# Kernel optimization log

Hardware: AMD Instinct MI355X
Metric: run time of the kernel (lower is better)

Reference implementation:

```python
import jax, jax.numpy as jnp
import numpy as np

B, T, D = 4, 4096, 768      # batch, tokens, n_embd
S = 1024                    # memory_slots (divides T -> adaptive pool == window mean)
K = 8                       # memory_topk
RW = 0.1                    # memory_retrieval_weight


def setup_inputs() -> dict:
    key = jax.random.key(0)
    ks = jax.random.split(key, 10)
    w = 1.0 / np.sqrt(D).astype(np.float32)
    return {
        "x": jax.random.normal(ks[0], (B, T, D), jnp.float32),
        "Wq": jax.random.normal(ks[1], (D, D), jnp.float32) * w,
        "bq": jnp.zeros((D,), jnp.float32),
        "Wk": jax.random.normal(ks[2], (D, D), jnp.float32) * w,
        "bk": jnp.zeros((D,), jnp.float32),
        "Wv": jax.random.normal(ks[3], (D, D), jnp.float32) * w,
        "bv": jnp.zeros((D,), jnp.float32),
        "Wp": jax.random.normal(ks[4], (D, D), jnp.float32) * w,
        "bp": jnp.zeros((D,), jnp.float32),
        "persistent_memory": jax.random.normal(ks[5], (S, D), jnp.float32),
    }


def reference(x, Wq, bq, Wk, bk, Wv, bv, Wp, bp, persistent_memory):
    # _build_memory_slots: adaptive_avg_pool1d to S slots; T % S == 0 so it is a window mean
    pooled = x.reshape(B, S, T // S, D).mean(axis=2)                    # [B,S,D]
    pers = jnp.broadcast_to(persistent_memory[None], (B, S, D))         # persistent bank
    slots = jnp.concatenate([pooled, pers], axis=1)                     # [B,2S,D]

    q = x @ Wq + bq                                                     # [B,T,D]
    k = slots @ Wk + bk                                                 # [B,2S,D]
    v = slots @ Wv + bv                                                 # [B,2S,D]

    scores = jnp.einsum('btd,bsd->bts', q, k) / jnp.sqrt(jnp.float32(D))  # [B,T,2S]
    top_s, top_i = jax.lax.top_k(scores, K)                             # [B,T,K]
    w = jax.nn.softmax(top_s, axis=-1)                                  # softmax over top-k only

    # gather top-k values: [B,T,K,D]
    vg = jnp.take_along_axis(v, top_i.reshape(B, T * K)[:, :, None], axis=1)
    vg = vg.reshape(B, T, K, D)
    retrieved = jnp.einsum('btk,btkd->btd', w, vg)                      # weighted combine

    return RW * (retrieved @ Wp + bp)                                   # proj * retrieval_weight
```

## Files before the change

kernel.cpp:

```cpp
#include <hip/hip_runtime.h>
#include <math.h>

#define BB 4
#define TT 4096
#define DD 768
#define SS 1024
#define S2 2048
#define KTOP 8
#define RWEIGHT 0.1f
#define TAU 2e-4f
#define AMB_CAP 128

typedef __attribute__((ext_vector_type(8))) _Float16 f16x8;
typedef __attribute__((ext_vector_type(4))) float f32x4;
typedef _Float16 f16;

__global__ __launch_bounds__(256) void build_pooled_all(
    const float* __restrict__ x, float* __restrict__ slots)
{
    int i = blockIdx.x * 256 + threadIdx.x;
    int s2 = i / DD;
    int d = i - s2 * DD;
    int b = s2 >> 10, s = s2 & 1023;
    const float* xb = x + (size_t)b * TT * DD + (size_t)(4 * s) * DD + d;
// ... 12 lines not shown
              : (blockIdx.z == 2) ? T2 : T3;
    __shared__ float t[32][33];
    int bx = blockIdx.x * 32, by = blockIdx.y * 32;
    int lx = threadIdx.x & 31, ly = threadIdx.x >> 5;
#pragma unroll
    for (int r = 0; r < 32; r += 8)
        t[ly + r][lx] = W[(size_t)(bx + ly + r) * 768 + by + lx];
    __syncthreads();
#pragma unroll
    for (int r = 0; r < 32; r += 8)
        WT[(size_t)(by + ly + r) * 768 + bx + lx] = t[lx][ly + r];
}

__global__ void zeroN(int* p) { p[threadIdx.x] = 0; }

__global__ __launch_bounds__(256) void producers(
    const float* __restrict__ xq, const float* __restrict__ aslots,
    const f16* __restrict__ aproj,
    const float* __restrict__ WqT, const float* __restrict__ WkT,
    const float* __restrict__ WvT, const float* __restrict__ WpT,
    const float* __restrict__ bq, const float* __restrict__ bk,
    const float* __restrict__ bv, const float* __restrict__ bp,
    f16* __restrict__ qh, f16* __restrict__ qm,
    f16* __restrict__ kh, f16* __restrict__ km,
    f16* __restrict__ v16, float* __restrict__ oproj,
    int n_q, int n_kv, int rowoff)
{
    __shared__ f16 LAh[4096], LAm[4096], LBh[4096], LBm[4096];
    const int tid = threadIdx.x;
    const int lane = tid & 63;
    const int wc = (tid >> 6) & 1;
    const int wr = (tid >> 7) & 1;

    int t = blockIdx.x, mode, bx, by;
    if (t < n_q) { mode = 0; bx = t % 6; by = t / 6; }
    else if (t < n_q + n_kv) { mode = 1; int u = t - n_q; bx = u % 6; by = u / 6; }
    else if (t < n_q + 2 * n_kv) { mode = 2; int u = t - n_q - n_kv; bx = u % 6; by = u / 6; }
    else { mode = 3; int u = t - n_q - 2 * n_kv; bx = u % 6; by = u / 6; }

    const int srow = tid >> 1, c0 = tid & 1;
    const int p0 = c0 ^ (srow & 3) ^ ((srow >> 2) & 1);
    const int wo0 = srow * 32 + p0 * 8, wo1 = wo0 ^ 16;
    const int csw = (((lane >> 4) ^ (lane & 3) ^ ((lane >> 2) & 1)) * 8);
    const int arow0 = by * 128;
    const size_t bn = (size_t)bx * 128;

    f32x4 acc[4][4];
#pragma unroll
    for (int i = 0; i < 4; ++i)
#pragma unroll
        for (int j = 0; j < 4; ++j) acc[i][j] = (f32x4){0.f, 0.f, 0.f, 0.f};

    const int orow0 = wr * 64 + (lane >> 4) * 4;
    const int ocol0 = wc * 64 + (lane & 15);

    if (mode <= 1) {
        const float* A  = (mode == 0) ? xq : aslots;
        const float* BT = (mode == 0) ? WqT : WkT;
        const float* bi = (mode == 0) ? bq : bk;
        f16* Ch = (mode == 0) ? qh : kh;
        f16* Cm = (mode == 0) ? qm : km;
        const int crow0 = ((mode == 0) ? 0 : rowoff) + arow0;
        const float* pa = A + (size_t)(arow0 + srow) * 768 + c0 * 8;
        const float* pb = BT + (bn + srow) * 768 + c0 * 8;

        for (int k0 = 0; k0 < 768; k0 += 32) {
            float4 a0 = *(const float4*)(pa + k0);
            float4 a1 = *(const float4*)(pa + k0 + 4);
            float4 a2 = *(const float4*)(pa + k0 + 16);
            float4 a3 = *(const float4*)(pa + k0 + 20);
            float4 b0 = *(const float4*)(pb + k0);
            float4 b1 = *(const float4*)(pb + k0 + 4);
            float4 b2 = *(const float4*)(pb + k0 + 16);
            float4 b3 = *(const float4*)(pb + k0 + 20);
            __syncthreads();
            {
                float av[16] = {a0.x, a0.y, a0.z, a0.w, a1.x, a1.y, a1.z, a1.w,
                                a2.x, a2.y, a2.z, a2.w, a3.x, a3.y, a3.z, a3.w};
                float bv2[16] = {b0.x, b0.y, b0.z, b0.w, b1.x, b1.y, b1.z, b1.w,
                                 b2.x, b2.y, b2.z, b2.w, b3.x, b3.y, b3.z, b3.w};
                f16x8 h, m;
#pragma unroll
                for (int j = 0; j < 8; ++j) {
                    f16 hh = (f16)av[j]; h[j] = hh; m[j] = (f16)(av[j] - (float)hh);
                }
                *(f16x8*)&LAh[wo0] = h; *(f16x8*)&LAm[wo0] = m;
#pragma unroll
                for (int j = 0; j < 8; ++j) {
                    f16 hh = (f16)av[j + 8]; h[j] = hh; m[j] = (f16)(av[j + 8] - (float)hh);
                }
                *(f16x8*)&LAh[wo1] = h; *(f16x8*)&LAm[wo1] = m;
#pragma unroll
                for (int j = 0; j < 8; ++j) {
                    f16 hh = (f16)bv2[j]; h[j] = hh; m[j] = (f16)(bv2[j] - (float)hh);
                }
                *(f16x8*)&LBh[wo0] = h; *(f16x8*)&LBm[wo0] = m;
#pragma unroll
                for (int j = 0; j < 8; ++j) {
                    f16 hh = (f16)bv2[j + 8]; h[j] = hh; m[j] = (f16)(bv2[j + 8] - (float)hh);
                }
                *(f16x8*)&LBh[wo1] = h; *(f16x8*)&LBm[wo1] = m;
            }
            __syncthreads();

            f16x8 fah[4], fam[4], fbh[4], fbm[4];
#pragma unroll
            for (int mi = 0; mi < 4; ++mi) {
                int off = (wr * 64 + mi * 16 + (lane & 15)) * 32 + csw;
                fah[mi] = *(const f16x8*)&LAh[off];
                fam[mi] = *(const f16x8*)&LAm[off];
            }
#pragma unroll
            for (int ni = 0; ni < 4; ++ni) {
                int off = (wc * 64 + ni * 16 + (lane & 15)) * 32 + csw;
                fbh[ni] = *(const f16x8*)&LBh[off];
                fbm[ni] = *(const f16x8*)&LBm[off];
            }
#pragma unroll
            for (int mi = 0; mi < 4; ++mi)
#pragma unroll
                for (int ni = 0; ni < 4; ++ni) {
                    acc[mi][ni] = __builtin_amdgcn_mfma_f32_16x16x32_f16(
                        fah[mi], fbh[ni], acc[mi][ni], 0, 0, 0);
                    acc[mi][ni] = __builtin_amdgcn_mfma_f32_16x16x32_f16(
                        fah[mi], fbm[ni], acc[mi][ni], 0, 0, 0);
                    acc[mi][ni] = __builtin_amdgcn_mfma_f32_16x16x32_f16(
                        fam[mi], fbh[ni], acc[mi][ni], 0, 0, 0);
                }
        }
#pragma unroll
        for (int mi = 0; mi < 4; ++mi)
#pragma unroll
            for (int ni = 0; ni < 4; ++ni) {
                size_t col = bn + ocol0 + ni * 16;
                float badd = bi[col];
                size_t rbase = (size_t)crow0 + orow0 + mi * 16;
#pragma unroll
                for (int r = 0; r < 4; ++r) {
                    float val = acc[mi][ni][r] + badd;
                    f16 h = (f16)val;
                    size_t idx = (rbase + r) * 768 + col;
                    Ch[idx] = h;
                    Cm[idx] = (f16)(val - (float)h);
                }
            }
    } else if (mode == 2) {
        const int crow0 = rowoff + arow0;
        const float* pa = aslots + (size_t)(arow0 + srow) * 768 + c0 * 8;
        const float* pb = WvT + (bn + srow) * 768 + c0 * 8;
        for (int k0 = 0; k0 < 768; k0 += 32) {
            float4 a0 = *(const float4*)(pa + k0);
            float4 a1 = *(const float4*)(pa + k0 + 4);
            float4 a2 = *(const float4*)(pa + k0 + 16);
            float4 a3 = *(const float4*)(pa + k0 + 20);
            float4 b0 = *(const float4*)(pb + k0);
            float4 b1 = *(const float4*)(pb + k0 + 4);
            float4 b2 = *(const float4*)(pb + k0 + 16);
            float4 b3 = *(const float4*)(pb + k0 + 20);
            __syncthreads();
            {
                f16x8 h;
                h[0] = (f16)a0.x; h[1] = (f16)a0.y; h[2] = (f16)a0.z; h[3] = (f16)a0.w;
                h[4] = (f16)a1.x; h[5] = (f16)a1.y; h[6] = (f16)a1.z; h[7] = (f16)a1.w;
                *(f16x8*)&LAh[wo0] = h;
                h[0] = (f16)a2.x; h[1] = (f16)a2.y; h[2] = (f16)a2.z; h[3] = (f16)a2.w;
                h[4] = (f16)a3.x; h[5] = (f16)a3.y; h[6] = (f16)a3.z; h[7] = (f16)a3.w;
                *(f16x8*)&LAh[wo1] = h;
                h[0] = (f16)b0.x; h[1] = (f16)b0.y; h[2] = (f16)b0.z; h[3] = (f16)b0.w;
                h[4] = (f16)b1.x; h[5] = (f16)b1.y; h[6] = (f16)b1.z; h[7] = (f16)b1.w;
                *(f16x8*)&LBh[wo0] = h;
                h[0] = (f16)b2.x; h[1] = (f16)b2.y; h[2] = (f16)b2.z; h[3] = (f16)b2.w;
                h[4] = (f16)b3.x; h[5] = (f16)b3.y; h[6] = (f16)b3.z; h[7] = (f16)b3.w;
                *(f16x8*)&LBh[wo1] = h;
            }
            __syncthreads();
            f16x8 fah[4], fbh[4];
#pragma unroll
            for (int mi = 0; mi < 4; ++mi)
                fah[mi] = *(const f16x8*)&LAh[(wr * 64 + mi * 16 + (lane & 15)) * 32 + csw];
#pragma unroll
            for (int ni = 0; ni < 4; ++ni)
                fbh[ni] = *(const f16x8*)&LBh[(wc * 64 + ni * 16 + (lane & 15)) * 32 + csw];
#pragma unroll
            for (int mi = 0; mi < 4; ++mi)
#pragma unroll
                for (int ni = 0; ni < 4; ++ni)
                    acc[mi][ni] = __builtin_amdgcn_mfma_f32_16x16x32_f16(
                        fah[mi], fbh[ni], acc[mi][ni], 0, 0, 0);
        }
#pragma unroll
        for (int mi = 0; mi < 4; ++mi)
#pragma unroll
            for (int ni = 0; ni < 4; ++ni) {
                size_t col = bn + ocol0 + ni * 16;
                float badd = bv[col];
                size_t rbase = (size_t)crow0 + orow0 + mi * 16;
#pragma unroll
                for (int r = 0; r < 4; ++r)
                    v16[(rbase + r) * 768 + col] = (f16)(acc[mi][ni][r] + badd);
            }
    } else {
        const f16* pa = aproj + (size_t)(arow0 + srow) * 768 + c0 * 8;
        const float* pb = WpT + (bn + srow) * 768 + c0 * 8;
        for (int k0 = 0; k0 < 768; k0 += 32) {
            f16x8 ah0 = *(const f16x8*)(pa + k0);
            f16x8 ah1 = *(const f16x8*)(pa + k0 + 16);
            float4 b0 = *(const float4*)(pb + k0);
            float4 b1 = *(const float4*)(pb + k0 + 4);
            float4 b2 = *(const float4*)(pb + k0 + 16);
            float4 b3 = *(const float4*)(pb + k0 + 20);
            __syncthreads();
            *(f16x8*)&LAh[wo0] = ah0;
            *(f16x8*)&LAh[wo1] = ah1;
            {
                f16x8 h;
                h[0] = (f16)b0.x; h[1] = (f16)b0.y; h[2] = (f16)b0.z; h[3] = (f16)b0.w;
                h[4] = (f16)b1.x; h[5] = (f16)b1.y; h[6] = (f16)b1.z; h[7] = (f16)b1.w;
                *(f16x8*)&LBh[wo0] = h;
                h[0] = (f16)b2.x; h[1] = (f16)b2.y; h[2] = (f16)b2.z; h[3] = (f16)b2.w;
                h[4] = (f16)b3.x; h[5] = (f16)b3.y; h[6] = (f16)b3.z; h[7] = (f16)b3.w;
                *(f16x8*)&LBh[wo1] = h;
            }
            __syncthreads();
            f16x8 fah[4], fbh[4];
#pragma unroll
            for (int mi = 0; mi < 4; ++mi)
                fah[mi] = *(const f16x8*)&LAh[(wr * 64 + mi * 16 + (lane & 15)) * 32 + csw];
#pragma unroll
            for (int ni = 0; ni < 4; ++ni)
                fbh[ni] = *(const f16x8*)&LBh[(wc * 64 + ni * 16 + (lane & 15)) * 32 + csw];
#pragma unroll
            for (int mi = 0; mi < 4; ++mi)
#pragma unroll
                for (int ni = 0; ni < 4; ++ni)
                    acc[mi][ni] = __builtin_amdgcn_mfma_f32_16x16x32_f16(
                        fah[mi], fbh[ni], acc[mi][ni], 0, 0, 0);
        }
#pragma unroll
        for (int mi = 0; mi < 4; ++mi)
#pragma unroll
            for (int ni = 0; ni < 4; ++ni) {
                size_t col = bn + ocol0 + ni * 16;
                float badd = RWEIGHT * bp[col];
                size_t rbase = (size_t)arow0 + orow0 + mi * 16;
#pragma unroll
                for (int r = 0; r < 4; ++r)
                    oproj[(rbase + r) * 768 + col] = RWEIGHT * acc[mi][ni][r] + badd;
            }
    }
}

__global__ __launch_bounds__(256) void scores_planes(
    const f16* __restrict__ qh, const f16* __restrict__ qm,
    const f16* __restrict__ kh, const f16* __restrict__ km,
    float* __restrict__ C, float alpha)
{
    __shared__ f16 LAh[4096], LAm[4096], LBh[4096], LBm[4096];
    const int tid = threadIdx.x;
    const int lane = tid & 63;
    const int wc = (tid >> 6) & 1;
    const int wr = (tid >> 7) & 1;
    const size_t bm = (size_t)blockIdx.y * 128;
    const size_t bn = (size_t)blockIdx.x * 128;

    f32x4 acc[4][4];
#pragma unroll
    for (int i = 0; i < 4; ++i)
#pragma unroll
        for (int j = 0; j < 4; ++j) acc[i][j] = (f32x4){0.f, 0.f, 0.f, 0.f};

    const int srow = tid >> 1, c0 = tid & 1;
    const int p0 = c0 ^ (srow & 3) ^ ((srow >> 2) & 1);
    const int wo0 = srow * 32 + p0 * 8, wo1 = wo0 ^ 16;
    const int csw = (((lane >> 4) ^ (lane & 3) ^ ((lane >> 2) & 1)) * 8);

    const f16* pah = qh + (bm + srow) * 768 + c0 * 8;
    const f16* pam = qm + (bm + srow) * 768 + c0 * 8;
    const f16* pbh = kh + (bn + srow) * 768 + c0 * 8;
    const f16* pbm = km + (bn + srow) * 768 + c0 * 8;

    for (int k0 = 0; k0 < 768; k0 += 32) {
        f16x8 ah0 = *(const f16x8*)(pah + k0);
        f16x8 ah1 = *(const f16x8*)(pah + k0 + 16);
        f16x8 am0 = *(const f16x8*)(pam + k0);
        f16x8 am1 = *(const f16x8*)(pam + k0 + 16);
        f16x8 bh0 = *(const f16x8*)(pbh + k0);
        f16x8 bh1 = *(const f16x8*)(pbh + k0 + 16);
        f16x8 bm0 = *(const f16x8*)(pbm + k0);
        f16x8 bm1 = *(const f16x8*)(pbm + k0 + 16);
        __syncthreads();
        *(f16x8*)&LAh[wo0] = ah0; *(f16x8*)&LAh[wo1] = ah1;
        *(f16x8*)&LAm[wo0] = am0; *(f16x8*)&LAm[wo1] = am1;
// ... 22 lines not shown
                    fah[mi], fbh[ni], acc[mi][ni], 0, 0, 0);
                acc[mi][ni] = __builtin_amdgcn_mfma_f32_16x16x32_f16(
                    fah[mi], fbm[ni], acc[mi][ni], 0, 0, 0);
                acc[mi][ni] = __builtin_amdgcn_mfma_f32_16x16x32_f16(
                    fam[mi], fbh[ni], acc[mi][ni], 0, 0, 0);
            }
    }

    const int orow0 = wr * 64 + (lane >> 4) * 4;
    const int ocol0 = wc * 64 + (lane & 15);
#pragma unroll
    for (int mi = 0; mi < 4; ++mi)
#pragma unroll
        for (int ni = 0; ni < 4; ++ni) {
            size_t col = bn + ocol0 + ni * 16;
            size_t rbase = bm + orow0 + mi * 16;
#pragma unroll
            for (int r = 0; r < 4; ++r)
                C[(rbase + r) * S2 + col] = alpha * acc[mi][ni][r];
        }
}

__global__ __launch_bounds__(256) void select_combine(
    const float* __restrict__ scores, const f16* __restrict__ v16,
    f16* __restrict__ retrc, int gbase,
    int* __restrict__ amb_count, int* __restrict__ amb_grow,
    int* __restrict__ cand, float* __restrict__ oldw, f16* __restrict__ vsave)
{
    const int lane = threadIdx.x & 63;
    const int wave = threadIdx.x >> 6;
    const int row = blockIdx.x * 4 + wave;

    const float* srow = scores + (size_t)row * S2;
    float vals[32];
#pragma unroll
    for (int i = 0; i < 32; ++i) vals[i] = srow[lane + (i << 6)];

    float topv[16]; int topi[16];
    bool amb = false;
    int nr = 9;
    for (int r = 0; r < 16; ++r) {
        if (r >= nr) break;
        float bvv = -3.4e38f; int bii = 0x7fffffff;
#pragma unroll
        for (int i = 0; i < 32; ++i)
            if (vals[i] > bvv) { bvv = vals[i]; bii = lane + (i << 6); }
#pragma unroll
        for (int off = 32; off > 0; off >>= 1) {
            float ov = __shfl_xor(bvv, off);
            int   oi = __shfl_xor(bii, off);
            if (ov > bvv || (ov == bvv && oi < bii)) { bvv = ov; bii = oi; }
        }
        topv[r] = bvv; topi[r] = bii;
        if ((bii & 63) == lane) vals[bii >> 6] = -3.4e38f;
        if (r == 8) {
            amb = (topv[7] - topv[8]) < TAU;
            if (amb) nr = 16;
        }
    }

    float m = topv[0], w[KTOP], sum = 0.f;
#pragma unroll
    for (int r = 0; r < KTOP; ++r) { w[r] = expf(topv[r] - m); sum += w[r]; }
    float inv = 1.f / sum;
#pragma unroll
    for (int r = 0; r < KTOP; ++r) w[r] *= inv;

    if (amb) {
        int idx = 0;
        if (lane == 0) idx = atomicAdd(amb_count, 1);
        idx = __shfl(idx, 0);
        if (idx < AMB_CAP) {
            if (lane == 0) amb_grow[idx] = gbase + row;
            if (lane < 16) cand[idx * 16 + lane] = topi[lane];
            if (lane < KTOP) oldw[idx * KTOP + lane] = w[lane];
            f16* vs = vsave + (size_t)idx * 16 * 768;
            for (int cc = lane; cc < 16 * 96; cc += 64) {
                int cr = cc / 96, ch = cc - cr * 96;
                *(f16x8*)&vs[(size_t)cr * 768 + ch * 8] =
                    *(const f16x8*)&v16[(size_t)topi[cr] * 768 + ch * 8];
            }
        }
    }

    for (int c = lane; c < 96; c += 64) {
        float o[8] = {0, 0, 0, 0, 0, 0, 0, 0};
#pragma unroll
        for (int r = 0; r < KTOP; ++r) {
            f16x8 vv = *(const f16x8*)&v16[(size_t)topi[r] * 768 + c * 8];
#pragma unroll
            for (int j = 0; j < 8; ++j) o[j] += w[r] * (float)vv[j];
        }
        f16x8 hx;
#pragma unroll
        for (int j = 0; j < 8; ++j) hx[j] = (f16)o[j];
        *(f16x8*)&retrc[(size_t)row * 768 + c * 8] = hx;
    }
}

__global__ __launch_bounds__(256) void fixA(
    const int* __restrict__ amb_count, const int* __restrict__ amb_grow,
    const float* __restrict__ x, const float* __restrict__ Wq,
    const float* __restrict__ bq, double* __restrict__ q64buf)
{
    int n = *amb_count; if (n > AMB_CAP) n = AMB_CAP;
    const int i = blockIdx.y;
    if (i >= n) return;
    const int tid = threadIdx.x;
    const int jl = tid & 63;
    const int ks = tid >> 6;
    const int j = blockIdx.x * 64 + jl;
    const int grow = amb_grow[i];
// ... 201 lines not shown
    const float inv_sqrt_d = (float)(1.0 / sqrt((double)DD));
    const size_t TD  = (size_t)TT * DD;
    const size_t SD  = (size_t)SS * DD;
    const size_t WSZ = (size_t)DD * DD;

    float* p = ws;
    float* WqT = p; p += WSZ;
    float* WkT = p; p += WSZ;
    float* WvT = p; p += WSZ;
    float* WpT = p; p += WSZ;
    float* slots_all = p; p += (size_t)BB * SD;
    f16* qh = (f16*)p; p += TD / 2;
    f16* qm = (f16*)p; p += TD / 2;
    f16* kh = (f16*)p; p += SD;
    f16* km = (f16*)p; p += SD;
    f16* v16 = (f16*)p; p += SD;
    f16* retrA = (f16*)p; p += TD / 2;
    f16* retrB = (f16*)p; p += TD / 2;
    double* q64buf = (double*)p; p += (size_t)AMB_CAP * DD * 2;
    double* ubuf   = (double*)p; p += (size_t)AMB_CAP * DD * 2;
    double* bkqbuf = (double*)p; p += AMB_CAP * 2;
    int* cand = (int*)p; p += (size_t)AMB_CAP * 16;
    float* oldw = p; p += (size_t)AMB_CAP * KTOP;
    f16* vsave = (f16*)p; p += (size_t)AMB_CAP * 16 * DD / 2;
    float* dret = p; p += (size_t)AMB_CAP * DD;
    int* ambc = (int*)p; p += 64;
    int* ambgrow = (int*)p; p += AMB_CAP;
    float* scores = p;
    size_t used = (size_t)(p - ws);

    long tc = TT;
    while (tc > 512 && (used + (size_t)tc * S2) * 4 > ws_size) tc >>= 1;

    transpose_all<<<dim3(24, 24, 4), 256, 0, stream>>>(
        Wq, Wk, Wv, Wp, WqT, WkT, WvT, WpT);
    zeroN<<<1, 64, 0, stream>>>(ambc);
    build_pooled_all<<<(BB * SS * DD) / 256, 256, 0, stream>>>(x, slots_all);

    producers<<<96, 256, 0, stream>>>(
        nullptr, pm, nullptr, WqT, WkT, WvT, WpT, bq, bk, bv, bp,
        qh, qm, kh, km, v16, nullptr, 0, 48, SS);

    for (int b = 0; b < BB; ++b) {
        const float* xb = x + (size_t)b * TD;
        const float* slots_b = slots_all + (size_t)b * SD;
        f16* rcur = (b & 1) ? retrB : retrA;
        f16* rprev = (b & 1) ? retrA : retrB;
        int np = b ? 192 : 0;

        producers<<<288 + np, 256, 0, stream>>>(
            xb, slots_b, rprev, WqT, WkT, WvT, WpT, bq, bk, bv, bp,
            qh, qm, kh, km, v16, out + (size_t)(b - 1) * TD, 192, 48, 0);

        for (long t0 = 0; t0 < TT; t0 += tc) {
            scores_planes<<<dim3(16, tc / 128), 256, 0, stream>>>(
                qh + (size_t)t0 * DD, qm + (size_t)t0 * DD, kh, km,
                scores, inv_sqrt_d);
            select_combine<<<tc / 4, 256, 0, stream>>>(
                scores, v16, rcur + (size_t)t0 * DD, b * TT + (int)t0,
                ambc, ambgrow, cand, oldw, vsave);
        }
    }

    f16* rlast = ((BB - 1) & 1) ? retrB : retrA;
    producers<<<192, 256, 0, stream>>>(
        nullptr, nullptr, rlast, WqT, WkT, WvT, WpT, bq, bk, bv, bp,
        qh, qm, kh, km, v16, out + (size_t)(BB - 1) * TD, 0, 0, 0);

    fixA<<<dim3(12, AMB_CAP), 256, 0, stream>>>(ambc, ambgrow, x, Wq, bq, q64buf);
    fixB<<<dim3(12, AMB_CAP), 256, 0, stream>>>(ambc, WkT, bk, q64buf, ubuf, bkqbuf);
    fixC<<<AMB_CAP, 256, 0, stream>>>(ambc, ambgrow, x, pm, cand, oldw,
                                      ubuf, bkqbuf, vsave, dret);
    fixD<<<dim3(12, AMB_CAP), 256, 0, stream>>>(ambc, ambgrow, dret, Wp, out);
}
```

Baseline: 648.5 us.

## Fuse select/combine with next-batch producers and scores with projection into mega-kernels

Splits the producer GEMM variants into device tile functions and builds two heterogeneous mega-kernels. One runs top-k selection and combine for batch b-1 alongside the Q/K/V producers for batch b. The other runs the score GEMM for batch b alongside the output projection of batch b-1. This software-pipelines the batches across fewer launches so independent work fills the GPU together. The V buffer is now double-buffered and the persistent-memory V is written to both copies. The adaptive chunking of the scores buffer by workspace size is removed, so the full T×2S scores buffer is now assumed to fit.

```diff
diff --git a/kernel.cpp b/kernel.cpp
--- a/kernel.cpp
+++ b/kernel.cpp
@@ -50,268 +50,297 @@
 
 __global__ void zeroN(int* p) { p[threadIdx.x] = 0; }
 
-__global__ __launch_bounds__(256) void producers(
-    const float* __restrict__ xq, const float* __restrict__ aslots,
-    const f16* __restrict__ aproj,
-    const float* __restrict__ WqT, const float* __restrict__ WkT,
-    const float* __restrict__ WvT, const float* __restrict__ WpT,
-    const float* __restrict__ bq, const float* __restrict__ bk,
-    const float* __restrict__ bv, const float* __restrict__ bp,
-    f16* __restrict__ qh, f16* __restrict__ qm,
-    f16* __restrict__ kh, f16* __restrict__ km,
-    f16* __restrict__ v16, float* __restrict__ oproj,
-    int n_q, int n_kv, int rowoff)
-{
-    __shared__ f16 LAh[4096], LAm[4096], LBh[4096], LBm[4096];
+__device__ __forceinline__ void tile_split_prod(
+    const float* __restrict__ A, int arow0,
+    const float* __restrict__ BT, int bncol,
+    const float* __restrict__ bias,
+    f16* __restrict__ Ch, f16* __restrict__ Cm, int crow0,
+    f16* LAh, f16* LAm, f16* LBh, f16* LBm)
+{
     const int tid = threadIdx.x;
     const int lane = tid & 63;
     const int wc = (tid >> 6) & 1;
     const int wr = (tid >> 7) & 1;
-
-    int t = blockIdx.x, mode, bx, by;
-    if (t < n_q) { mode = 0; bx = t % 6; by = t / 6; }
-    else if (t < n_q + n_kv) { mode = 1; int u = t - n_q; bx = u % 6; by = u / 6; }
-    else if (t < n_q + 2 * n_kv) { mode = 2; int u = t - n_q - n_kv; bx = u % 6; by = u / 6; }
-    else { mode = 3; int u = t - n_q - 2 * n_kv; bx = u % 6; by = u / 6; }
-
     const int srow = tid >> 1, c0 = tid & 1;
     const int p0 = c0 ^ (srow & 3) ^ ((srow >> 2) & 1);
     const int wo0 = srow * 32 + p0 * 8, wo1 = wo0 ^ 16;
     const int csw = (((lane >> 4) ^ (lane & 3) ^ ((lane >> 2) & 1)) * 8);
-    const int arow0 = by * 128;
-    const size_t bn = (size_t)bx * 128;
+    const size_t bn = (size_t)bncol;
 
     f32x4 acc[4][4];
 #pragma unroll
     for (int i = 0; i < 4; ++i)
 #pragma unroll
         for (int j = 0; j < 4; ++j) acc[i][j] = (f32x4){0.f, 0.f, 0.f, 0.f};
+
+    const float* pa = A + (size_t)(arow0 + srow) * 768 + c0 * 8;
+    const float* pb = BT + (bn + srow) * 768 + c0 * 8;
+
+    for (int k0 = 0; k0 < 768; k0 += 32) {
+        float4 a0 = *(const float4*)(pa + k0);
+        float4 a1 = *(const float4*)(pa + k0 + 4);
+        float4 a2 = *(const float4*)(pa + k0 + 16);
+        float4 a3 = *(const float4*)(pa + k0 + 20);
+        float4 b0 = *(const float4*)(pb + k0);
+        float4 b1 = *(const float4*)(pb + k0 + 4);
+        float4 b2 = *(const float4*)(pb + k0 + 16);
+        float4 b3 = *(const float4*)(pb + k0 + 20);
+        __syncthreads();
+        {
+            float av[16] = {a0.x, a0.y, a0.z, a0.w, a1.x, a1.y, a1.z, a1.w,
+                            a2.x, a2.y, a2.z, a2.w, a3.x, a3.y, a3.z, a3.w};
+            float bv2[16] = {b0.x, b0.y, b0.z, b0.w, b1.x, b1.y, b1.z, b1.w,
+                             b2.x, b2.y, b2.z, b2.w, b3.x, b3.y, b3.z, b3.w};
+            f16x8 h, m;
+#pragma unroll
+            for (int j = 0; j < 8; ++j) {
+                f16 hh = (f16)av[j]; h[j] = hh; m[j] = (f16)(av[j] - (float)hh);
+            }
+            *(f16x8*)&LAh[wo0] = h; *(f16x8*)&LAm[wo0] = m;
+#pragma unroll
+            for (int j = 0; j < 8; ++j) {
+                f16 hh = (f16)av[j + 8]; h[j] = hh; m[j] = (f16)(av[j + 8] - (float)hh);
+            }
+            *(f16x8*)&LAh[wo1] = h; *(f16x8*)&LAm[wo1] = m;
+#pragma unroll
+            for (int j = 0; j < 8; ++j) {
+                f16 hh = (f16)bv2[j]; h[j] = hh; m[j] = (f16)(bv2[j] - (float)hh);
+            }
+            *(f16x8*)&LBh[wo0] = h; *(f16x8*)&LBm[wo0] = m;
+#pragma unroll
+            for (int j = 0; j < 8; ++j) {
+                f16 hh = (f16)bv2[j + 8]; h[j] = hh; m[j] = (f16)(bv2[j + 8] - (float)hh);
+            }
+            *(f16x8*)&LBh[wo1] = h; *(f16x8*)&LBm[wo1] = m;
+        }
+        __syncthreads();
+
+        f16x8 fah[4], fam[4], fbh[4], fbm[4];
+#pragma unroll
+        for (int mi = 0; mi < 4; ++mi) {
+            int off = (wr * 64 + mi * 16 + (lane & 15)) * 32 + csw;
+            fah[mi] = *(const f16x8*)&LAh[off];
+            fam[mi] = *(const f16x8*)&LAm[off];
+        }
+#pragma unroll
+        for (int ni = 0; ni < 4; ++ni) {
+            int off = (wc * 64 + ni * 16 + (lane & 15)) * 32 + csw;
+            fbh[ni] = *(const f16x8*)&LBh[off];
+            fbm[ni] = *(const f16x8*)&LBm[off];
+        }
+#pragma unroll
+        for (int mi = 0; mi < 4; ++mi)
+#pragma unroll
+            for (int ni = 0; ni < 4; ++ni) {
+                acc[mi][ni] = __builtin_amdgcn_mfma_f32_16x16x32_f16(
+                    fah[mi], fbh[ni], acc[mi][ni], 0, 0, 0);
+                acc[mi][ni] = __builtin_amdgcn_mfma_f32_16x16x32_f16(
+                    fah[mi], fbm[ni], acc[mi][ni], 0, 0, 0);
+                acc[mi][ni] = __builtin_amdgcn_mfma_f32_16x16x32_f16(
+                    fam[mi], fbh[ni], acc[mi][ni], 0, 0, 0);
+            }
+    }
 
     const int orow0 = wr * 64 + (lane >> 4) * 4;
     const int ocol0 = wc * 64 + (lane & 15);
-
-    if (mode <= 1) {
-        const float* A  = (mode == 0) ? xq : aslots;
-        const float* BT = (mode == 0) ? WqT : WkT;
-        const float* bi = (mode == 0) ? bq : bk;
-        f16* Ch = (mode == 0) ? qh : kh;
-        f16* Cm = (mode == 0) ? qm : km;
-        const int crow0 = ((mode == 0) ? 0 : rowoff) + arow0;
-        const float* pa = A + (size_t)(arow0 + srow) * 768 + c0 * 8;
-        const float* pb = BT + (bn + srow) * 768 + c0 * 8;
-
-        for (int k0 = 0; k0 < 768; k0 += 32) {
-            float4 a0 = *(const float4*)(pa + k0);
-            float4 a1 = *(const float4*)(pa + k0 + 4);
-            float4 a2 = *(const float4*)(pa + k0 + 16);
-            float4 a3 = *(const float4*)(pa + k0 + 20);
-            float4 b0 = *(const float4*)(pb + k0);
-            float4 b1 = *(const float4*)(pb + k0 + 4);
-            float4 b2 = *(const float4*)(pb + k0 + 16);
-            float4 b3 = *(const float4*)(pb + k0 + 20);
-            __syncthreads();
-            {
-                float av[16] = {a0.x, a0.y, a0.z, a0.w, a1.x, a1.y, a1.z, a1.w,
-                                a2.x, a2.y, a2.z, a2.w, a3.x, a3.y, a3.z, a3.w};
-                float bv2[16] = {b0.x, b0.y, b0.z, b0.w, b1.x, b1.y, b1.z, b1.w,
-                                 b2.x, b2.y, b2.z, b2.w, b3.x, b3.y, b3.z, b3.w};
-                f16x8 h, m;
-#pragma unroll
-                for (int j = 0; j < 8; ++j) {
-                    f16 hh = (f16)av[j]; h[j] = hh; m[j] = (f16)(av[j] - (float)hh);
-                }
-                *(f16x8*)&LAh[wo0] = h; *(f16x8*)&LAm[wo0] = m;
-#pragma unroll
-                for (int j = 0; j < 8; ++j) {
-                    f16 hh = (f16)av[j + 8]; h[j] = hh; m[j] = (f16)(av[j + 8] - (float)hh);
-                }
-                *(f16x8*)&LAh[wo1] = h; *(f16x8*)&LAm[wo1] = m;
-#pragma unroll
-                for (int j = 0; j < 8; ++j) {
-                    f16 hh = (f16)bv2[j]; h[j] = hh; m[j] = (f16)(bv2[j] - (float)hh);
-                }
-                *(f16x8*)&LBh[wo0] = h; *(f16x8*)&LBm[wo0] = m;
-#pragma unroll
-                for (int j = 0; j < 8; ++j) {
-                    f16 hh = (f16)bv2[j + 8]; h[j] = hh; m[j] = (f16)(bv2[j + 8] - (float)hh);
-                }
-                *(f16x8*)&LBh[wo1] = h; *(f16x8*)&LBm[wo1] = m;
-            }
-            __syncthreads();
-
-            f16x8 fah[4], fam[4], fbh[4], fbm[4];
-#pragma unroll
-            for (int mi = 0; mi < 4; ++mi) {
-                int off = (wr * 64 + mi * 16 + (lane & 15)) * 32 + csw;
-                fah[mi] = *(const f16x8*)&LAh[off];
-                fam[mi] = *(const f16x8*)&LAm[off];
-            }
-#pragma unroll
-            for (int ni = 0; ni < 4; ++ni) {
-                int off = (wc * 64 + ni * 16 + (lane & 15)) * 32 + csw;
-                fbh[ni] = *(const f16x8*)&LBh[off];
-                fbm[ni] = *(const f16x8*)&LBm[off];
-            }
-#pragma unroll
-            for (int mi = 0; mi < 4; ++mi)
-#pragma unroll
-                for (int ni = 0; ni < 4; ++ni) {
-                    acc[mi][ni] = __builtin_amdgcn_mfma_f32_16x16x32_f16(
-                        fah[mi], fbh[ni], acc[mi][ni], 0, 0, 0);
-                    acc[mi][ni] = __builtin_amdgcn_mfma_f32_16x16x32_f16(
-                        fah[mi], fbm[ni], acc[mi][ni], 0, 0, 0);
-                    acc[mi][ni] = __builtin_amdgcn_mfma_f32_16x16x32_f16(
-                        fam[mi], fbh[ni], acc[mi][ni], 0, 0, 0);
-                }
-        }
-#pragma unroll
-        for (int mi = 0; mi < 4; ++mi)
-#pragma unroll
-            for (int ni = 0; ni < 4; ++ni) {
-                size_t col = bn + ocol0 + ni * 16;
-                float badd = bi[col];
-                size_t rbase = (size_t)crow0 + orow0 + mi * 16;
-#pragma unroll
-                for (int r = 0; r < 4; ++r) {
-                    float val = acc[mi][ni][r] + badd;
-                    f16 h = (f16)val;
-                    size_t idx = (rbase + r) * 768 + col;
-                    Ch[idx] = h;
-                    Cm[idx] = (f16)(val - (float)h);
-                }
-            }
-    } else if (mode == 2) {
-        const int crow0 = rowoff + arow0;
-        const float* pa = aslots + (size_t)(arow0 + srow) * 768 + c0 * 8;
-        const float* pb = WvT + (bn + srow) * 768 + c0 * 8;
-        for (int k0 = 0; k0 < 768; k0 += 32) {
-            float4 a0 = *(const float4*)(pa + k0);
-            float4 a1 = *(const float4*)(pa + k0 + 4);
-            float4 a2 = *(const float4*)(pa + k0 + 16);
-            float4 a3 = *(const float4*)(pa + k0 + 20);
-            float4 b0 = *(const float4*)(pb + k0);
-            float4 b1 = *(const float4*)(pb + k0 + 4);
-            float4 b2 = *(const float4*)(pb + k0 + 16);
-            float4 b3 = *(const float4*)(pb + k0 + 20);
-            __syncthreads();
-            {
-                f16x8 h;
-                h[0] = (f16)a0.x; h[1] = (f16)a0.y; h[2] = (f16)a0.z; h[3] = (f16)a0.w;
-                h[4] = (f16)a1.x; h[5] = (f16)a1.y; h[6] = (f16)a1.z; h[7] = (f16)a1.w;
-                *(f16x8*)&LAh[wo0] = h;
-                h[0] = (f16)a2.x; h[1] = (f16)a2.y; h[2] = (f16)a2.z; h[3] = (f16)a2.w;
-                h[4] = (f16)a3.x; h[5] = (f16)a3.y; h[6] = (f16)a3.z; h[7] = (f16)a3.w;
-                *(f16x8*)&LAh[wo1] = h;
-                h[0] = (f16)b0.x; h[1] = (f16)b0.y; h[2] = (f16)b0.z; h[3] = (f16)b0.w;
-                h[4] = (f16)b1.x; h[5] = (f16)b1.y; h[6] = (f16)b1.z; h[7] = (f16)b1.w;
-                *(f16x8*)&LBh[wo0] = h;
-                h[0] = (f16)b2.x; h[1] = (f16)b2.y; h[2] = (f16)b2.z; h[3] = (f16)b2.w;
-                h[4] = (f16)b3.x; h[5] = (f16)b3.y; h[6] = (f16)b3.z; h[7] = (f16)b3.w;
-                *(f16x8*)&LBh[wo1] = h;
-            }
-            __syncthreads();
-            f16x8 fah[4], fbh[4];
-#pragma unroll
-            for (int mi = 0; mi < 4; ++mi)
-                fah[mi] = *(const f16x8*)&LAh[(wr * 64 + mi * 16 + (lane & 15)) * 32 + csw];
-#pragma unroll
-            for (int ni = 0; ni < 4; ++ni)
-                fbh[ni] = *(const f16x8*)&LBh[(wc * 64 + ni * 16 + (lane & 15)) * 32 + csw];
-#pragma unroll
-            for (int mi = 0; mi < 4; ++mi)
-#pragma unroll
-                for (int ni = 0; ni < 4; ++ni)
-                    acc[mi][ni] = __builtin_amdgcn_mfma_f32_16x16x32_f16(
-                        fah[mi], fbh[ni], acc[mi][ni], 0, 0, 0);
-        }
-#pragma unroll
-        for (int mi = 0; mi < 4; ++mi)
-#pragma unroll
-            for (int ni = 0; ni < 4; ++ni) {
-                size_t col = bn + ocol0 + ni * 16;
-                float badd = bv[col];
-                size_t rbase = (size_t)crow0 + orow0 + mi * 16;
-#pragma unroll
-                for (int r = 0; r < 4; ++r)
-                    v16[(rbase + r) * 768 + col] = (f16)(acc[mi][ni][r] + badd);
-            }
-    } else {
-        const f16* pa = aproj + (size_t)(arow0 + srow) * 768 + c0 * 8;
-        const float* pb = WpT + (bn + srow) * 768 + c0 * 8;
-        for (int k0 = 0; k0 < 768; k0 += 32) {
-            f16x8 ah0 = *(const f16x8*)(pa + k0);
-            f16x8 ah1 = *(const f16x8*)(pa + k0 + 16);
-            float4 b0 = *(const float4*)(pb + k0);
-            float4 b1 = *(const float4*)(pb + k0 + 4);
-            float4 b2 = *(const float4*)(pb + k0 + 16);
-            float4 b3 = *(const float4*)(pb + k0 + 20);
-            __syncthreads();
-            *(f16x8*)&LAh[wo0] = ah0;
-            *(f16x8*)&LAh[wo1] = ah1;
-            {
-                f16x8 h;
-                h[0] = (f16)b0.x; h[1] = (f16)b0.y; h[2] = (f16)b0.z; h[3] = (f16)b0.w;
-                h[4] = (f16)b1.x; h[5] = (f16)b1.y; h[6] = (f16)b1.z; h[7] = (f16)b1.w;
-                *(f16x8*)&LBh[wo0] = h;
-                h[0] = (f16)b2.x; h[1] = (f16)b2.y; h[2] = (f16)b2.z; h[3] = (f16)b2.w;
-                h[4] = (f16)b3.x; h[5] = (f16)b3.y; h[6] = (f16)b3.z; h[7] = (f16)b3.w;
-                *(f16x8*)&LBh[wo1] = h;
-            }
-            __syncthreads();
-            f16x8 fah[4], fbh[4];
-#pragma unroll
-            for (int mi = 0; mi < 4; ++mi)
-                fah[mi] = *(const f16x8*)&LAh[(wr * 64 + mi * 16 + (lane & 15)) * 32 + csw];
-#pragma unroll
-            for (int ni = 0; ni < 4; ++ni)
-                fbh[ni] = *(const f16x8*)&LBh[(wc * 64 + ni * 16 + (lane & 15)) * 32 + csw];
-#pragma unroll
-            for (int mi = 0; mi < 4; ++mi)
-#pragma unroll
-                for (int ni = 0; ni < 4; ++ni)
-                    acc[mi][ni] = __builtin_amdgcn_mfma_f32_16x16x32_f16(
-                        fah[mi], fbh[ni], acc[mi][ni], 0, 0, 0);
-        }
-#pragma unroll
-        for (int mi = 0; mi < 4; ++mi)
-#pragma unroll
-            for (int ni = 0; ni < 4; ++ni) {
-                size_t col = bn + ocol0 + ni * 16;
-                float badd = RWEIGHT * bp[col];
-                size_t rbase = (size_t)arow0 + orow0 + mi * 16;
-#pragma unroll
-                for (int r = 0; r < 4; ++r)
-                    oproj[(rbase + r) * 768 + col] = RWEIGHT * acc[mi][ni][r] + badd;
-            }
-    }
-}
-
-__global__ __launch_bounds__(256) void scores_planes(
-    const f16* __restrict__ qh, const f16* __restrict__ qm,
-    const f16* __restrict__ kh, const f16* __restrict__ km,
-    float* __restrict__ C, float alpha)
-{
-    __shared__ f16 LAh[4096], LAm[4096], LBh[4096], LBm[4096];
+#pragma unroll
+    for (int mi = 0; mi < 4; ++mi)
+#pragma unroll
+        for (int ni = 0; ni < 4; ++ni) {
+            size_t col = bn + ocol0 + ni * 16;
+            float badd = bias[col];
+            size_t rbase = (size_t)crow0 + orow0 + mi * 16;
+#pragma unroll
+            for (int r = 0; r < 4; ++r) {
+                float val = acc[mi][ni][r] + badd;
+                f16 h = (f16)val;
+                size_t idx = (rbase + r) * 768 + col;
+                Ch[idx] = h;
+                Cm[idx] = (f16)(val - (float)h);
+            }
+        }
+}
+
+__device__ __forceinline__ void tile_f32A_f16O(
+    const float* __restrict__ A, int arow0,
+    const float* __restrict__ BT, int bncol,
+    const float* __restrict__ bias,
+    f16* __restrict__ Co, int crow0, f16* LA, f16* LB)
+{
     const int tid = threadIdx.x;
     const int lane = tid & 63;
     const int wc = (tid >> 6) & 1;
     const int wr = (tid >> 7) & 1;
-    const size_t bm = (size_t)blockIdx.y * 128;
-    const size_t bn = (size_t)blockIdx.x * 128;
-
-    f32x4 acc[4][4];
-#pragma unroll
-    for (int i = 0; i < 4; ++i)
-#pragma unroll
-        for (int j = 0; j < 4; ++j) acc[i][j] = (f32x4){0.f, 0.f, 0.f, 0.f};
-
     const int srow = tid >> 1, c0 = tid & 1;
     const int p0 = c0 ^ (srow & 3) ^ ((srow >> 2) & 1);
     const int wo0 = srow * 32 + p0 * 8, wo1 = wo0 ^ 16;
     const int csw = (((lane >> 4) ^ (lane & 3) ^ ((lane >> 2) & 1)) * 8);
-
-    const f16* pah = qh + (bm + srow) * 768 + c0 * 8;
-    const f16* pam = qm + (bm + srow) * 768 + c0 * 8;
+    const size_t bn = (size_t)bncol;
+
+    f32x4 acc[4][4];
+#pragma unroll
+    for (int i = 0; i < 4; ++i)
+#pragma unroll
+        for (int j = 0; j < 4; ++j) acc[i][j] = (f32x4){0.f, 0.f, 0.f, 0.f};
+
+    const float* pa = A + (size_t)(arow0 + srow) * 768 + c0 * 8;
+    const float* pb = BT + (bn + srow) * 768 + c0 * 8;
+
+    for (int k0 = 0; k0 < 768; k0 += 32) {
+        float4 a0 = *(const float4*)(pa + k0);
+        float4 a1 = *(const float4*)(pa + k0 + 4);
+        float4 a2 = *(const float4*)(pa + k0 + 16);
+        float4 a3 = *(const float4*)(pa + k0 + 20);
+        float4 b0 = *(const float4*)(pb + k0);
+        float4 b1 = *(const float4*)(pb + k0 + 4);
+        float4 b2 = *(const float4*)(pb + k0 + 16);
+        float4 b3 = *(const float4*)(pb + k0 + 20);
+        __syncthreads();
+        {
+            f16x8 h;
+            h[0] = (f16)a0.x; h[1] = (f16)a0.y; h[2] = (f16)a0.z; h[3] = (f16)a0.w;
+            h[4] = (f16)a1.x; h[5] = (f16)a1.y; h[6] = (f16)a1.z; h[7] = (f16)a1.w;
+            *(f16x8*)&LA[wo0] = h;
+            h[0] = (f16)a2.x; h[1] = (f16)a2.y; h[2] = (f16)a2.z; h[3] = (f16)a2.w;
+            h[4] = (f16)a3.x; h[5] = (f16)a3.y; h[6] = (f16)a3.z; h[7] = (f16)a3.w;
+            *(f16x8*)&LA[wo1] = h;
+            h[0] = (f16)b0.x; h[1] = (f16)b0.y; h[2] = (f16)b0.z; h[3] = (f16)b0.w;
+            h[4] = (f16)b1.x; h[5] = (f16)b1.y; h[6] = (f16)b1.z; h[7] = (f16)b1.w;
+            *(f16x8*)&LB[wo0] = h;
+            h[0] = (f16)b2.x; h[1] = (f16)b2.y; h[2] = (f16)b2.z; h[3] = (f16)b2.w;
+            h[4] = (f16)b3.x; h[5] = (f16)b3.y; h[6] = (f16)b3.z; h[7] = (f16)b3.w;
+            *(f16x8*)&LB[wo1] = h;
+        }
+        __syncthreads();
+        f16x8 fah[4], fbh[4];
+#pragma unroll
+        for (int mi = 0; mi < 4; ++mi)
+            fah[mi] = *(const f16x8*)&LA[(wr * 64 + mi * 16 + (lane & 15)) * 32 + csw];
+#pragma unroll
+        for (int ni = 0; ni < 4; ++ni)
+            fbh[ni] = *(const f16x8*)&LB[(wc * 64 + ni * 16 + (lane & 15)) * 32 + csw];
+#pragma unroll
+        for (int mi = 0; mi < 4; ++mi)
+#pragma unroll
+            for (int ni = 0; ni < 4; ++ni)
+                acc[mi][ni] = __builtin_amdgcn_mfma_f32_16x16x32_f16(
+                    fah[mi], fbh[ni], acc[mi][ni], 0, 0, 0);
+    }
+
+    const int orow0 = wr * 64 + (lane >> 4) * 4;
+    const int ocol0 = wc * 64 + (lane & 15);
+#pragma unroll
+    for (int mi = 0; mi < 4; ++mi)
+#pragma unroll
+        for (int ni = 0; ni < 4; ++ni) {
+            size_t col = bn + ocol0 + ni * 16;
+            float badd = bias[col];
+            size_t rbase = (size_t)crow0 + orow0 + mi * 16;
+#pragma unroll
+            for (int r = 0; r < 4; ++r)
+                Co[(rbase + r) * 768 + col] = (f16)(acc[mi][ni][r] + badd);
+        }
+}
+
+__device__ __forceinline__ void tile_f16A_f32O(
+    const f16* __restrict__ A, int arow0,
+    const float* __restrict__ BT, int bncol,
+    const float* __restrict__ bias,
+    float* __restrict__ Co, int crow0, f16* LA, f16* LB)
+{
+    const int tid = threadIdx.x;
+    const int lane = tid & 63;
+    const int wc = (tid >> 6) & 1;
+    const int wr = (tid >> 7) & 1;
+    const int srow = tid >> 1, c0 = tid & 1;
+    const int p0 = c0 ^ (srow & 3) ^ ((srow >> 2) & 1);
+    const int wo0 = srow * 32 + p0 * 8, wo1 = wo0 ^ 16;
+    const int csw = (((lane >> 4) ^ (lane & 3) ^ ((lane >> 2) & 1)) * 8);
+    const size_t bn = (size_t)bncol;
+
+    f32x4 acc[4][4];
+#pragma unroll
+    for (int i = 0; i < 4; ++i)
+#pragma unroll
+        for (int j = 0; j < 4; ++j) acc[i][j] = (f32x4){0.f, 0.f, 0.f, 0.f};
+
+    const f16* pa = A + (size_t)(arow0 + srow) * 768 + c0 * 8;
+    const float* pb = BT + (bn + srow) * 768 + c0 * 8;
+
+    for (int k0 = 0; k0 < 768; k0 += 32) {
+        f16x8 ah0 = *(const f16x8*)(pa + k0);
+        f16x8 ah1 = *(const f16x8*)(pa + k0 + 16);
+        float4 b0 = *(const float4*)(pb + k0);
+        float4 b1 = *(const float4*)(pb + k0 + 4);
+        float4 b2 = *(const float4*)(pb + k0 + 16);
+        float4 b3 = *(const float4*)(pb + k0 + 20);
+        __syncthreads();
+        *(f16x8*)&LA[wo0] = ah0;
+        *(f16x8*)&LA[wo1] = ah1;
+        {
+            f16x8 h;
+            h[0] = (f16)b0.x; h[1] = (f16)b0.y; h[2] = (f16)b0.z; h[3] = (f16)b0.w;
+            h[4] = (f16)b1.x; h[5] = (f16)b1.y; h[6] = (f16)b1.z; h[7] = (f16)b1.w;
+            *(f16x8*)&LB[wo0] = h;
+            h[0] = (f16)b2.x; h[1] = (f16)b2.y; h[2] = (f16)b2.z; h[3] = (f16)b2.w;
+            h[4] = (f16)b3.x; h[5] = (f16)b3.y; h[6] = (f16)b3.z; h[7] = (f16)b3.w;
+            *(f16x8*)&LB[wo1] = h;
+        }
+        __syncthreads();
+        f16x8 fah[4], fbh[4];
+#pragma unroll
+        for (int mi = 0; mi < 4; ++mi)
+            fah[mi] = *(const f16x8*)&LA[(wr * 64 + mi * 16 + (lane & 15)) * 32 + csw];
+#pragma unroll
+        for (int ni = 0; ni < 4; ++ni)
+            fbh[ni] = *(const f16x8*)&LB[(wc * 64 + ni * 16 + (lane & 15)) * 32 + csw];
+#pragma unroll
+        for (int mi = 0; mi < 4; ++mi)
+#pragma unroll
+            for (int ni = 0; ni < 4; ++ni)
+                acc[mi][ni] = __builtin_amdgcn_mfma_f32_16x16x32_f16(
+                    fah[mi], fbh[ni], acc[mi][ni], 0, 0, 0);
+    }
+
+    const int orow0 = wr * 64 + (lane >> 4) * 4;
+    const int ocol0 = wc * 64 + (lane & 15);
+#pragma unroll
+    for (int mi = 0; mi < 4; ++mi)
+#pragma unroll
+        for (int ni = 0; ni < 4; ++ni) {
+            size_t col = bn + ocol0 + ni * 16;
+            float badd = RWEIGHT * bias[col];
+            size_t rbase = (size_t)crow0 + orow0 + mi * 16;
+#pragma unroll
+            for (int r = 0; r < 4; ++r)
+                Co[(rbase + r) * 768 + col] = RWEIGHT * acc[mi][ni][r] + badd;
+        }
+}
+
+__device__ __forceinline__ void tile_scores_planes(
+    const f16* __restrict__ qh, const f16* __restrict__ qm, int arow0,
+    const f16* __restrict__ kh, const f16* __restrict__ km, int bncol,
+    float* __restrict__ C, float alpha,
+    f16* LAh, f16* LAm, f16* LBh, f16* LBm)
+{
+    const int tid = threadIdx.x;
+    const int lane = tid & 63;
+    const int wc = (tid >> 6) & 1;
+    const int wr = (tid >> 7) & 1;
+    const int srow = tid >> 1, c0 = tid & 1;
+    const int p0 = c0 ^ (srow & 3) ^ ((srow >> 2) & 1);
+    const int wo0 = srow * 32 + p0 * 8, wo1 = wo0 ^ 16;
+    const int csw = (((lane >> 4) ^ (lane & 3) ^ ((lane >> 2) & 1)) * 8);
+    const size_t bn = (size_t)bncol;
+
+    f32x4 acc[4][4];
+#pragma unroll
+    for (int i = 0; i < 4; ++i)
+#pragma unroll
+        for (int j = 0; j < 4; ++j) acc[i][j] = (f32x4){0.f, 0.f, 0.f, 0.f};
+
+    const f16* pah = qh + (size_t)(arow0 + srow) * 768 + c0 * 8;
+    const f16* pam = qm + (size_t)(arow0 + srow) * 768 + c0 * 8;
     const f16* pbh = kh + (bn + srow) * 768 + c0 * 8;
     const f16* pbm = km + (bn + srow) * 768 + c0 * 8;
 
@@ -364,88 +393,163 @@
 #pragma unroll
         for (int ni = 0; ni < 4; ++ni) {
             size_t col = bn + ocol0 + ni * 16;
-            size_t rbase = bm + orow0 + mi * 16;
+            size_t rbase = (size_t)arow0 + orow0 + mi * 16;
 #pragma unroll
             for (int r = 0; r < 4; ++r)
                 C[(rbase + r) * S2 + col] = alpha * acc[mi][ni][r];
         }
 }
 
-__global__ __launch_bounds__(256) void select_combine(
-    const float* __restrict__ scores, const f16* __restrict__ v16,
-    f16* __restrict__ retrc, int gbase,
-    int* __restrict__ amb_count, int* __restrict__ amb_grow,
-    int* __restrict__ cand, float* __restrict__ oldw, f16* __restrict__ vsave)
-{
-    const int lane = threadIdx.x & 63;
-    const int wave = threadIdx.x >> 6;
-    const int row = blockIdx.x * 4 + wave;
-
-    const float* srow = scores + (size_t)row * S2;
-    float vals[32];
-#pragma unroll
-    for (int i = 0; i < 32; ++i) vals[i] = srow[lane + (i << 6)];
-
-    float topv[16]; int topi[16];
-    bool amb = false;
-    int nr = 9;
-    for (int r = 0; r < 16; ++r) {
-        if (r >= nr) break;
-        float bvv = -3.4e38f; int bii = 0x7fffffff;
-#pragma unroll
-        for (int i = 0; i < 32; ++i)
-            if (vals[i] > bvv) { bvv = vals[i]; bii = lane + (i << 6); }
-#pragma unroll
-        for (int off = 32; off > 0; off >>= 1) {
-            float ov = __shfl_xor(bvv, off);
-            int   oi = __shfl_xor(bii, off);
-            if (ov > bvv || (ov == bvv && oi < bii)) { bvv = ov; bii = oi; }
-        }
-        topv[r] = bvv; topi[r] = bii;
-        if ((bii & 63) == lane) vals[bii >> 6] = -3.4e38f;
-        if (r == 8) {
-            amb = (topv[7] - topv[8]) < TAU;
-            if (amb) nr = 16;
-        }
-    }
-
-    float m = topv[0], w[KTOP], sum = 0.f;
-#pragma unroll
-    for (int r = 0; r < KTOP; ++r) { w[r] = expf(topv[r] - m); sum += w[r]; }
-    float inv = 1.f / sum;
-#pragma unroll
-    for (int r = 0; r < KTOP; ++r) w[r] *= inv;
-
-    if (amb) {
-        int idx = 0;
-        if (lane == 0) idx = atomicAdd(amb_count, 1);
-        idx = __shfl(idx, 0);
-        if (idx < AMB_CAP) {
-            if (lane == 0) amb_grow[idx] = gbase + row;
-            if (lane < 16) cand[idx * 16 + lane] = topi[lane];
-            if (lane < KTOP) oldw[idx * KTOP + lane] = w[lane];
-            f16* vs = vsave + (size_t)idx * 16 * 768;
-            for (int cc = lane; cc < 16 * 96; cc += 64) {
-                int cr = cc / 96, ch = cc - cr * 96;
-                *(f16x8*)&vs[(size_t)cr * 768 + ch * 8] =
-                    *(const f16x8*)&v16[(size_t)topi[cr] * 768 + ch * 8];
-            }
-        }
-    }
-
-    for (int c = lane; c < 96; c += 64) {
-        float o[8] = {0, 0, 0, 0, 0, 0, 0, 0};
-#pragma unroll
-        for (int r = 0; r < KTOP; ++r) {
-            f16x8 vv = *(const f16x8*)&v16[(size_t)topi[r] * 768 + c * 8];
-#pragma unroll
-            for (int j = 0; j < 8; ++j) o[j] += w[r] * (float)vv[j];
-        }
-        f16x8 hx;
-#pragma unroll
-        for (int j = 0; j < 8; ++j) hx[j] = (f16)o[j];
-        *(f16x8*)&retrc[(size_t)row * 768 + c * 8] = hx;
-    }
+__global__ __launch_bounds__(256) void megaSelProd(
+    int nSel, const float* __restrict__ scores, const f16* __restrict__ v16r,
+    f16* __restrict__ retrW, int gbase,
+    int* __restrict__ ambc, int* __restrict__ ambgrow, int* __restrict__ cand,
+    float* __restrict__ oldw, f16* __restrict__ vsave,
+    int hasQ, int hasKV, int doPm,
+    const float* __restrict__ xq, const float* __restrict__ slots_b,
+    const float* __restrict__ pm,
+    const float* __restrict__ WqT, const float* __restrict__ WkT,
+    const float* __restrict__ WvT,
+    const float* __restrict__ bq, const float* __restrict__ bk,
+    const float* __restrict__ bv,
+    f16* __restrict__ qh, f16* __restrict__ qm,
+    f16* __restrict__ kh, f16* __restrict__ km,
+    f16* __restrict__ v16w, f16* __restrict__ v16w2)
+{
+    __shared__ f16 LAh[4096], LAm[4096], LBh[4096], LBm[4096];
+    int t = blockIdx.x;
+
+    if (t < nSel) {
+        const int lane = threadIdx.x & 63;
+        const int wave = threadIdx.x >> 6;
+        const int row = t * 4 + wave;
+        const float* srow = scores + (size_t)row * S2;
+        float vals[32];
+#pragma unroll
+        for (int i = 0; i < 32; ++i) vals[i] = srow[lane + (i << 6)];
+
+        float topv[16]; int topi[16];
+        bool amb = false;
+        int nr = 9;
+        for (int r = 0; r < 16; ++r) {
+            if (r >= nr) break;
+            float bvv = -3.4e38f; int bii = 0x7fffffff;
+#pragma unroll
+            for (int i = 0; i < 32; ++i)
+                if (vals[i] > bvv) { bvv = vals[i]; bii = lane + (i << 6); }
+#pragma unroll
+            for (int off = 32; off > 0; off >>= 1) {
+                float ov = __shfl_xor(bvv, off);
+                int   oi = __shfl_xor(bii, off);
+                if (ov > bvv || (ov == bvv && oi < bii)) { bvv = ov; bii = oi; }
+            }
+            topv[r] = bvv; topi[r] = bii;
+            if ((bii & 63) == lane) vals[bii >> 6] = -3.4e38f;
+            if (r == 8) {
+                amb = (topv[7] - topv[8]) < TAU;
+                if (amb) nr = 16;
+            }
+        }
+
+        float m = topv[0], w[KTOP], sum = 0.f;
+#pragma unroll
+        for (int r = 0; r < KTOP; ++r) { w[r] = expf(topv[r] - m); sum += w[r]; }
+        float inv = 1.f / sum;
+#pragma unroll
+        for (int r = 0; r < KTOP; ++r) w[r] *= inv;
+
+        if (amb) {
+            int idx = 0;
+            if (lane == 0) idx = atomicAdd(ambc, 1);
+            idx = __shfl(idx, 0);
+            if (idx < AMB_CAP) {
+                if (lane == 0) ambgrow[idx] = gbase + row;
+                if (lane < 16) cand[idx * 16 + lane] = topi[lane];
+                if (lane < KTOP) oldw[idx * KTOP + lane] = w[lane];
+                f16* vs = vsave + (size_t)idx * 16 * 768;
+                for (int cc = lane; cc < 16 * 96; cc += 64) {
+                    int cr = cc / 96, ch = cc - cr * 96;
+                    *(f16x8*)&vs[(size_t)cr * 768 + ch * 8] =
+                        *(const f16x8*)&v16r[(size_t)topi[cr] * 768 + ch * 8];
+                }
+            }
+        }
+
+        for (int c = lane; c < 96; c += 64) {
+            float o[8] = {0, 0, 0, 0, 0, 0, 0, 0};
+#pragma unroll
+            for (int r = 0; r < KTOP; ++r) {
+                f16x8 vv = *(const f16x8*)&v16r[(size_t)topi[r] * 768 + c * 8];
+#pragma unroll
+                for (int j = 0; j < 8; ++j) o[j] += w[r] * (float)vv[j];
+            }
+            f16x8 hx;
+#pragma unroll
+            for (int j = 0; j < 8; ++j) hx[j] = (f16)o[j];
+            *(f16x8*)&retrW[(size_t)row * 768 + c * 8] = hx;
+        }
+        return;
+    }
+    t -= nSel;
+
+    if (hasQ) {
+        if (t < 192) {
+            tile_split_prod(xq, (t / 6) * 128, WqT, (t % 6) * 128, bq,
+                            qh, qm, (t / 6) * 128, LAh, LAm, LBh, LBm);
+            return;
+        }
+        t -= 192;
+    }
+    if (!hasKV) return;
+    if (t < 48) {
+        tile_split_prod(slots_b, (t / 6) * 128, WkT, (t % 6) * 128, bk,
+                        kh, km, (t / 6) * 128, LAh, LAm, LBh, LBm);
+        return;
+    }
+    t -= 48;
+    if (doPm) {
+        if (t < 48) {
+            tile_split_prod(pm, (t / 6) * 128, WkT, (t % 6) * 128, bk,
+                            kh, km, 1024 + (t / 6) * 128, LAh, LAm, LBh, LBm);
+            return;
+        }
+        t -= 48;
+    }
+    if (t < 48) {
+        tile_f32A_f16O(slots_b, (t / 6) * 128, WvT, (t % 6) * 128, bv,
+                       v16w, (t / 6) * 128, LAh, LBh);
+        return;
+    }
+    t -= 48;
+    if (doPm) {
+        if (t < 48) {
+            tile_f32A_f16O(pm, (t / 6) * 128, WvT, (t % 6) * 128, bv,
+                           v16w, 1024 + (t / 6) * 128, LAh, LBh);
+            return;
+        }
+        t -= 48;
+        tile_f32A_f16O(pm, (t / 6) * 128, WvT, (t % 6) * 128, bv,
+                       v16w2, 1024 + (t / 6) * 128, LAh, LBh);
+    }
+}
+
+__global__ __launch_bounds__(256) void megaScoresProj(
+    int nSc, const f16* __restrict__ qh, const f16* __restrict__ qm,
+    const f16* __restrict__ kh, const f16* __restrict__ km,
+    float* __restrict__ scores, float alpha,
+    const f16* __restrict__ retrR, const float* __restrict__ WpT,
+    const float* __restrict__ bp, float* __restrict__ outp)
+{
+    __shared__ f16 LAh[4096], LAm[4096], LBh[4096], LBm[4096];
+    int t = blockIdx.x;
+    if (t < nSc) {
+        tile_scores_planes(qh, qm, (t >> 4) * 128, kh, km, (t & 15) * 128,
+                           scores, alpha, LAh, LAm, LBh, LBm);
+        return;
+    }
+    t -= nSc;
+    tile_f16A_f32O(retrR, (t / 6) * 128, WpT, (t % 6) * 128, bp,
+                   outp, (t / 6) * 128, LAh, LBh);
 }
 
 __global__ __launch_bounds__(256) void fixA(
@@ -677,7 +781,8 @@
     f16* qm = (f16*)p; p += TD / 2;
     f16* kh = (f16*)p; p += SD;
     f16* km = (f16*)p; p += SD;
-    f16* v16 = (f16*)p; p += SD;
+    f16* v16a = (f16*)p; p += SD;
+    f16* v16b = (f16*)p; p += SD;
     f16* retrA = (f16*)p; p += TD / 2;
     f16* retrB = (f16*)p; p += TD / 2;
     double* q64buf = (double*)p; p += (size_t)AMB_CAP * DD * 2;
@@ -690,45 +795,44 @@
     int* ambc = (int*)p; p += 64;
     int* ambgrow = (int*)p; p += AMB_CAP;
     float* scores = p;
-    size_t used = (size_t)(p - ws);
-
-    long tc = TT;
-    while (tc > 512 && (used + (size_t)tc * S2) * 4 > ws_size) tc >>= 1;
 
     transpose_all<<<dim3(24, 24, 4), 256, 0, stream>>>(
         Wq, Wk, Wv, Wp, WqT, WkT, WvT, WpT);
     zeroN<<<1, 64, 0, stream>>>(ambc);
     build_pooled_all<<<(BB * SS * DD) / 256, 256, 0, stream>>>(x, slots_all);
 
-    producers<<<96, 256, 0, stream>>>(
-        nullptr, pm, nullptr, WqT, WkT, WvT, WpT, bq, bk, bv, bp,
-        qh, qm, kh, km, v16, nullptr, 0, 48, SS);
-
-    for (int b = 0; b < BB; ++b) {
-        const float* xb = x + (size_t)b * TD;
-        const float* slots_b = slots_all + (size_t)b * SD;
-        f16* rcur = (b & 1) ? retrB : retrA;
-        f16* rprev = (b & 1) ? retrA : retrB;
-        int np = b ? 192 : 0;
-
-        producers<<<288 + np, 256, 0, stream>>>(
-            xb, slots_b, rprev, WqT, WkT, WvT, WpT, bq, bk, bv, bp,
-            qh, qm, kh, km, v16, out + (size_t)(b - 1) * TD, 192, 48, 0);
-
-        for (long t0 = 0; t0 < TT; t0 += tc) {
-            scores_planes<<<dim3(16, tc / 128), 256, 0, stream>>>(
-                qh + (size_t)t0 * DD, qm + (size_t)t0 * DD, kh, km,
-                scores, inv_sqrt_d);
-            select_combine<<<tc / 4, 256, 0, stream>>>(
-                scores, v16, rcur + (size_t)t0 * DD, b * TT + (int)t0,
-                ambc, ambgrow, cand, oldw, vsave);
-        }
-    }
-
-    f16* rlast = ((BB - 1) & 1) ? retrB : retrA;
-    producers<<<192, 256, 0, stream>>>(
-        nullptr, nullptr, rlast, WqT, WkT, WvT, WpT, bq, bk, bv, bp,
-        qh, qm, kh, km, v16, out + (size_t)(BB - 1) * TD, 0, 0, 0);
+    megaSelProd<<<432, 256, 0, stream>>>(
+        0, nullptr, nullptr, nullptr, 0, ambc, ambgrow, cand, oldw, vsave,
+        1, 1, 1, x, slots_all, pm,
+        WqT, WkT, WvT, bq, bk, bv, qh, qm, kh, km, v16a, v16b);
+    megaScoresProj<<<512, 256, 0, stream>>>(
+        512, qh, qm, kh, km, scores, inv_sqrt_d, nullptr, WpT, bp, nullptr);
+
+    for (int b = 1; b < BB; ++b) {
+        f16* v16w = (b & 1) ? v16b : v16a;
+        f16* v16r = ((b - 1) & 1) ? v16b : v16a;
+        f16* retrW = ((b - 1) & 1) ? retrB : retrA;
+
+        megaSelProd<<<1312, 256, 0, stream>>>(
+            1024, scores, v16r, retrW, (b - 1) * TT,
+            ambc, ambgrow, cand, oldw, vsave,
+            1, 1, 0, x + (size_t)b * TD, slots_all + (size_t)b * SD, nullptr,
+            WqT, WkT, WvT, bq, bk, bv, qh, qm, kh, km, v16w, nullptr);
+        megaScoresProj<<<704, 256, 0, stream>>>(
+            512, qh, qm, kh, km, scores, inv_sqrt_d,
+            retrW, WpT, bp, out + (size_t)(b - 1) * TD);
+    }
+
+    f16* v16r3 = v16b;
+    f16* retrW3 = retrB;
+    megaSelProd<<<1024, 256, 0, stream>>>(
+        1024, scores, v16r3, retrW3, 3 * TT,
+        ambc, ambgrow, cand, oldw, vsave,
+        0, 0, 0, nullptr, nullptr, nullptr,
+        WqT, WkT, WvT, bq, bk, bv, qh, qm, kh, km, nullptr, nullptr);
+    megaScoresProj<<<192, 256, 0, stream>>>(
+        0, nullptr, nullptr, nullptr, nullptr, nullptr, 0.f,
+        retrW3, WpT, bp, out + (size_t)3 * TD);
 
     fixA<<<dim3(12, AMB_CAP), 256, 0, stream>>>(ambc, ambgrow, x, Wq, bq, q64buf);
     fixB<<<dim3(12, AMB_CAP), 256, 0, stream>>>(ambc, WkT, bk, q64buf, ubuf, bkqbuf);
```

Result: no change. 656.1 us (+1.2%).
